# Performance work log

Hardware: AMD Instinct MI355X
Metric: run time of the kernel (lower is better)

Reference implementation:

```python
import jax, jax.numpy as jnp
import numpy as np

N, H, D, G = 8192, 512, 256, 64
TAU, LAM, ALPHA, BETA = 0.5, 0.5, 1.0, 1.0
EPS_G, EPS_L = 1e-6, 1e-5


def setup_inputs() -> dict:
    key = jax.random.key(0)
    ks = jax.random.split(key, 8)
    za = jax.random.normal(ks[0], (N, H), dtype=jnp.float32)
    zb = jax.random.normal(ks[1], (N, H), dtype=jnp.float32)
    pos = jax.random.uniform(ks[2], (N, N), dtype=jnp.float32)
    batch = (jnp.arange(N, dtype=jnp.int32) * G) // N  # sorted, covers all G groups
    s_h = np.sqrt(2.0 / H).astype(np.float32)  # kaiming fan_in relu
    W1 = jax.random.normal(ks[3], (H, H), dtype=jnp.float32) * s_h
    b1 = jnp.zeros((H,), dtype=jnp.float32)
    W2 = jax.random.normal(ks[4], (H, H), dtype=jnp.float32) * s_h
    b2 = jnp.zeros((H,), dtype=jnp.float32)
    W3 = jax.random.normal(ks[5], (H, D), dtype=jnp.float32) * s_h
    b3 = jnp.zeros((D,), dtype=jnp.float32)
    a1 = jnp.full((1,), 0.5, dtype=jnp.float32)
    g1 = jnp.ones((H,), dtype=jnp.float32)
    be1 = jnp.zeros((H,), dtype=jnp.float32)
    a2 = jnp.full((1,), 0.5, dtype=jnp.float32)
    g2 = jnp.ones((H,), dtype=jnp.float32)
    be2 = jnp.zeros((H,), dtype=jnp.float32)
    return {"za": za, "zb": zb, "pos": pos, "batch": batch,
            "W1": W1, "b1": b1, "a1": a1, "g1": g1, "be1": be1,
            "W2": W2, "b2": b2, "a2": a2, "g2": g2, "be2": be2,
            "W3": W3, "b3": b3}


def _project(z, W1, b1, a1, g1, be1, W2, b2, a2, g2, be2, W3, b3):
    h = z @ W1 + b1
    h = jnp.tanh(a1 * h) * g1 + be1  # DyT
    h = h @ W2 + b2
    h = jnp.tanh(a2 * h) * g2 + be2  # DyT
    p = h @ W3 + b3
    return p * jax.nn.sigmoid(p)  # z1_proj * sigmoid(z1_proj)


def reference(za, zb, pos, batch, W1, b1, a1, g1, be1, W2, b2, a2, g2, be2, W3, b3):
    za_p = _project(za, W1, b1, a1, g1, be1, W2, b2, a2, g2, be2, W3, b3)
    zb_p = _project(zb, W1, b1, a1, g1, be1, W2, b2, a2, g2, be2, W3, b3)

    # exp(cosine / tau): same matrix used by global_contrast (sim) and local_contrast
    na = jnp.linalg.norm(za_p, axis=-1, keepdims=True)  # [N,1]
    nb = jnp.linalg.norm(zb_p, axis=-1, keepdims=True)  # [N,1]
    m = jnp.exp((za_p @ zb_p.T) / (na * nb.T) / TAU)    # [N,N]

    # global contrast
    a2b = m / (jnp.sum(m, axis=1, keepdims=True) + EPS_G)
    lori_a = -jnp.mean(jnp.log(jnp.sum(a2b * pos, axis=-1)))
    b2a = m.T
    b2a = b2a / (jnp.sum(b2a, axis=1, keepdims=True) + EPS_G)
    lori_b = -jnp.mean(jnp.log(jnp.sum(b2a * pos, axis=-1)))
    global_loss = LAM * lori_a + (1.0 - LAM) * lori_b

    # local contrast: per-group sums via one-hot matmul (replaces O(G^2) mask loop)
    pos_sim = jnp.diagonal(m)                              # [N]
    pos_sim_graph = jax.ops.segment_sum(pos_sim, batch, num_segments=G)  # [G]
    hot = jax.nn.one_hot(batch, G, dtype=m.dtype)          # [N,G]
    batch_sim = hot.T @ m @ hot                            # [G,G]
    graph_sim = jnp.diagonal(batch_sim)
    neg0 = jnp.sum(batch_sim, axis=0) - graph_sim
    neg1 = jnp.sum(batch_sim, axis=1) - graph_sim
    loss0 = jnp.mean(jnp.log(pos_sim_graph / (neg0 + EPS_L)))
    loss1 = jnp.mean(jnp.log(pos_sim_graph / (neg1 + EPS_L)))
    inter_loss = (loss0 + loss1) / 2.0
    inner_loss = -jnp.mean(jnp.log(pos_sim_graph / (graph_sim - pos_sim_graph + EPS_L)))
    local_loss = ALPHA * inter_loss + BETA * inner_loss

    total_loss = global_loss + local_loss
    return total_loss, jnp.concatenate((za_p, zb_p), axis=1)
```

## Files before the change

### kernel.cpp

```cpp
#include <hip/hip_runtime.h>
#include <hip/hip_bf16.h>
#include <cstdint>
#include <cstddef>


typedef __bf16 bf16;
typedef __bf16 bf16x4 __attribute__((ext_vector_type(4)));
typedef __bf16 bf16x8 __attribute__((ext_vector_type(8)));
typedef float  f32x4  __attribute__((ext_vector_type(4)));

#define NROWS 8192
#define HDIM  512
#define DDIM  256
#define GGRP  64
#define INV_TAU 2.0f

__device__ __forceinline__ void async_ld16(const void* g, void* l) {
    __builtin_amdgcn_global_load_lds(
        (__attribute__((address_space(1))) void*)(g),
        (__attribute__((address_space(3))) void*)(l), 16, 0, 0);
}

__device__ __forceinline__ void mfma_tile_128(
    const bf16* __restrict__ A, const bf16* __restrict__ Bt, int K,
    int row0, int col0, bf16* ldsA, bf16* ldsB, f32x4 acc[4][4])
{
    const int tid  = threadIdx.x;
    const int lane = tid & 63;
    const int wave = tid >> 6;
    const int wrow = (wave >> 1) * 64;
    const int wcol = (wave & 1) * 64;
    const int lrow = lane & 15;
    const int lk8  = (lane >> 4) * 8;

#pragma unroll
    for (int i = 0; i < 4; i++)
#pragma unroll
        for (int j = 0; j < 4; j++) acc[i][j] = (f32x4){0.f, 0.f, 0.f, 0.f};

    for (int k0 = 0; k0 < K; k0 += 32) {
#pragma unroll
        for (int t = 0; t < 2; t++) {
            int f = t * 256 + tid;
            int r = f >> 2;
            int c = (f & 3) * 8;
            async_ld16(A  + (size_t)(row0 + r) * K + k0 + c,
                       ldsA + (size_t)(t * 256 + wave * 64) * 8);
            async_ld16(Bt + (size_t)(col0 + r) * K + k0 + c,
                       ldsB + (size_t)(t * 256 + wave * 64) * 8);
        }
        __syncthreads();

        bf16x8 af[4], bfr[4];
#pragma unroll
        for (int fi = 0; fi < 4; fi++)
            af[fi] = *(const bf16x8*)(ldsA + (wrow + fi * 16 + lrow) * 32 + lk8);
#pragma unroll
        for (int fj = 0; fj < 4; fj++)
            bfr[fj] = *(const bf16x8*)(ldsB + (wcol + fj * 16 + lrow) * 32 + lk8);
#pragma unroll
        for (int fi = 0; fi < 4; fi++)
#pragma unroll
            for (int fj = 0; fj < 4; fj++)
                acc[fi][fj] = __builtin_amdgcn_mfma_f32_16x16x32_bf16(
                    af[fi], bfr[fj], acc[fi][fj], 0, 0, 0);
        __syncthreads();
    }
}

__global__ __launch_bounds__(256) void gemm_dyt(
    const bf16* __restrict__ A, const bf16* __restrict__ Bt, bf16* __restrict__ C,
    int K, int N,
    const float* __restrict__ bias, const float* __restrict__ alph,
    const float* __restrict__ gam, const float* __restrict__ bet)
{
    __shared__ __align__(16) bf16 ldsA[128 * 32];
    __shared__ __align__(16) bf16 ldsB[128 * 32];
    f32x4 acc[4][4];
    const int row0 = blockIdx.y * 128, col0 = blockIdx.x * 128;
    mfma_tile_128(A, Bt, K, row0, col0, ldsA, ldsB, acc);

    const int lane = threadIdx.x & 63, wave = threadIdx.x >> 6;
    const int wrow = (wave >> 1) * 64, wcol = (wave & 1) * 64;
    const int lcol = lane & 15, lrg = (lane >> 4) * 4;
    const float a = alph[0];
#pragma unroll
    for (int fi = 0; fi < 4; fi++) {
        const int rbase = row0 + wrow + fi * 16 + lrg;
#pragma unroll
        for (int fj = 0; fj < 4; fj++) {
            const int cg = col0 + wcol + fj * 16 + lcol;
            const float bcol = bias[cg], gcol = gam[cg], becol = bet[cg];
#pragma unroll
            for (int r = 0; r < 4; r++) {
                float x = acc[fi][fj][r] + bcol;
                float y = tanhf(a * x) * gcol + becol;
                C[(size_t)(rbase + r) * N + cg] = (bf16)y;
            }
        }
    }
}

__global__ __launch_bounds__(256) void gemm_silu(
    const bf16* __restrict__ A, const bf16* __restrict__ Bt,
    bf16* __restrict__ P16, float* __restrict__ out1, float* __restrict__ n2,
    const float* __restrict__ bias)
{
    __shared__ __align__(16) bf16 ldsA[128 * 32];
    __shared__ __align__(16) bf16 ldsB[128 * 32];
    f32x4 acc[4][4];
    const int row0 = blockIdx.y * 128, col0 = blockIdx.x * 128;
    mfma_tile_128(A, Bt, 512, row0, col0, ldsA, ldsB, acc);

    const int lane = threadIdx.x & 63, wave = threadIdx.x >> 6;
    const int wrow = (wave >> 1) * 64, wcol = (wave & 1) * 64;
    const int lcol = lane & 15, lrg = (lane >> 4) * 4;

    float nacc[4][4];
#pragma unroll
    for (int i = 0; i < 4; i++)
#pragma unroll
        for (int r = 0; r < 4; r++) nacc[i][r] = 0.f;

#pragma unroll
    for (int fi = 0; fi < 4; fi++) {
        const int rbase = row0 + wrow + fi * 16 + lrg;
#pragma unroll
        for (int fj = 0; fj < 4; fj++) {
            const int cg = col0 + wcol + fj * 16 + lcol;
            const float bcol = bias[cg];
#pragma unroll
            for (int r = 0; r < 4; r++) {
                const int rg = rbase + r;
                float x = acc[fi][fj][r] + bcol;
                float y = x / (1.f + __expf(-x));
                P16[(size_t)rg * 256 + cg] = (bf16)y;
                size_t oidx = (rg < NROWS) ? ((size_t)rg * 512 + cg)
                                           : ((size_t)(rg - NROWS) * 512 + 256 + cg);
                out1[oidx] = y;
                nacc[fi][r] += y * y;
            }
        }
    }
#pragma unroll
    for (int fi = 0; fi < 4; fi++)
#pragma unroll
        for (int r = 0; r < 4; r++) {
            float v = nacc[fi][r];
            v += __shfl_xor(v, 1); v += __shfl_xor(v, 2);
            v += __shfl_xor(v, 4); v += __shfl_xor(v, 8);
            if (lcol == 0)
                atomicAdd(&n2[row0 + wrow + fi * 16 + lrg + r], v);
        }
}

template <int PASS1>
__global__ __launch_bounds__(256, 2) void flash_sim(
    const bf16* __restrict__ PA, const bf16* __restrict__ PB,
    const float* __restrict__ rnA, const float* __restrict__ rnB,
    const float* __restrict__ pos,
    float* __restrict__ rsum, float* __restrict__ wsum,
    float* __restrict__ bsim, float* __restrict__ psg)
{
    const int lane = threadIdx.x & 63;
    const int wave = threadIdx.x >> 6;
    const int lrow = lane & 15;
    const int lk8  = (lane >> 4) * 8;
    const int lrg  = lane >> 4;
    const int R0   = blockIdx.y * 128 + wave * 32;
    const int C0   = blockIdx.x * 1024;

    bf16x8 a[2][8];
#pragma unroll
    for (int fi = 0; fi < 2; fi++)
#pragma unroll
        for (int kk = 0; kk < 8; kk++)
            a[fi][kk] = *(const bf16x8*)(
                PA + (size_t)(R0 + fi * 16 + lrow) * DDIM + kk * 32 + lk8);

    float rna[2][4];
#pragma unroll
    for (int fi = 0; fi < 2; fi++)
#pragma unroll
        for (int r = 0; r < 4; r++)
            rna[fi][r] = rnA[R0 + fi * 16 + lrg * 4 + r] * INV_TAU;

    float racc[2][4], sacc[2][4];
#pragma unroll
    for (int fi = 0; fi < 2; fi++)
#pragma unroll
        for (int r = 0; r < 4; r++) { racc[fi][r] = 0.f; sacc[fi][r] = 0.f; }
    float msum = 0.f, dacc = 0.f;

#pragma unroll 2
    for (int ct = 0; ct < 32; ct++) {
        const int c0 = C0 + ct * 32;

        bf16x8 b[2][8];
#pragma unroll
        for (int fj = 0; fj < 2; fj++)
#pragma unroll
            for (int kk = 0; kk < 8; kk++)
                b[fj][kk] = *(const bf16x8*)(
                    PB + (size_t)(c0 + fj * 16 + lrow) * DDIM + kk * 32 + lk8);

        f32x4 acc[2][2];
#pragma unroll
        for (int fi = 0; fi < 2; fi++)
#pragma unroll
            for (int fj = 0; fj < 2; fj++) acc[fi][fj] = (f32x4){0.f, 0.f, 0.f, 0.f};
#pragma unroll
        for (int kk = 0; kk < 8; kk++)
#pragma unroll
            for (int fi = 0; fi < 2; fi++)
#pragma unroll
                for (int fj = 0; fj < 2; fj++)
                    acc[fi][fj] = __builtin_amdgcn_mfma_f32_16x16x32_bf16(
                        a[fi][kk], b[fj][kk], acc[fi][fj], 0, 0, 0);

        float rnb[2];
        rnb[0] = rnB[c0 + lrow];
        rnb[1] = rnB[c0 + 16 + lrow];

        const bool diag_tile = PASS1 && (c0 == R0);
#pragma unroll
        for (int fi = 0; fi < 2; fi++)
#pragma unroll
            for (int fj = 0; fj < 2; fj++)
#pragma unroll
                for (int r = 0; r < 4; r++) {
                    float m = __expf(acc[fi][fj][r] * rna[fi][r] * rnb[fj]);
                    float pv = pos[(size_t)(R0 + fi * 16 + lrg * 4 + r) * NROWS
                                   + c0 + fj * 16 + lrow];
                    racc[fi][r] += m;
                    sacc[fi][r] += m * pv;
                    if (PASS1) {
                        msum += m;
                        if (diag_tile &&
                            (fi * 16 + lrg * 4 + r) == (fj * 16 + lrow))
                            dacc += m;
                    }
                }

        if (PASS1 && (ct & 3) == 3) {
            float v = msum;
            v += __shfl_xor(v, 1);  v += __shfl_xor(v, 2);
            v += __shfl_xor(v, 4);  v += __shfl_xor(v, 8);
            v += __shfl_xor(v, 16); v += __shfl_xor(v, 32);
            if (lane == 0)
                atomicAdd(&bsim[blockIdx.y * GGRP + (c0 >> 7)], v);
            msum = 0.f;
        }
    }

#pragma unroll
    for (int fi = 0; fi < 2; fi++)
#pragma unroll
        for (int r = 0; r < 4; r++) {
            float rv = racc[fi][r], sv = sacc[fi][r];
            rv += __shfl_xor(rv, 1); rv += __shfl_xor(rv, 2);
            rv += __shfl_xor(rv, 4); rv += __shfl_xor(rv, 8);
            sv += __shfl_xor(sv, 1); sv += __shfl_xor(sv, 2);
            sv += __shfl_xor(sv, 4); sv += __shfl_xor(sv, 8);
            if (lrow == 0) {
                const int rg = R0 + fi * 16 + lrg * 4 + r;
                atomicAdd(&rsum[rg], rv);
                atomicAdd(&wsum[rg], sv);
            }
        }
    if (PASS1 && blockIdx.x == (unsigned)(R0 >> 10)) {
        dacc += __shfl_xor(dacc, 1);  dacc += __shfl_xor(dacc, 2);
        dacc += __shfl_xor(dacc, 4);  dacc += __shfl_xor(dacc, 8);
        dacc += __shfl_xor(dacc, 16); dacc += __shfl_xor(dacc, 32);
        if (lane == 0) atomicAdd(&psg[blockIdx.y], dacc);
    }
}

__global__ void cast4_kernel(const float4* __restrict__ x, bf16x4* __restrict__ y, int n4)
{
    int i = blockIdx.x * blockDim.x + threadIdx.x;
    if (i < n4) {
        float4 v = x[i];
        bf16x4 o;
        o[0] = (bf16)v.x; o[1] = (bf16)v.y; o[2] = (bf16)v.z; o[3] = (bf16)v.w;
        y[i] = o;
    }
}

__global__ void transpose_cast(const float* __restrict__ W, bf16* __restrict__ Wt,
                               int R, int C)
{
    __shared__ float tile[32][33];
    const int c0 = blockIdx.x * 32, r0 = blockIdx.y * 32;
    const int tx = threadIdx.x, ty = threadIdx.y;
    for (int i = ty; i < 32; i += 8)
        tile[i][tx] = W[(size_t)(r0 + i) * C + c0 + tx];
    __syncthreads();
    for (int i = ty; i < 32; i += 8)
        Wt[(size_t)(c0 + i) * R + r0 + tx] = (bf16)tile[tx][i];
}

__global__ void rsqrt_kernel(const float* __restrict__ x, float* __restrict__ y, int n)
{
    int i = blockIdx.x * blockDim.x + threadIdx.x;
    if (i < n) y[i] = rsqrtf(fmaxf(x[i], 1e-30f));
}

__global__ void loss_kernel(
    const float* __restrict__ rowsum, const float* __restrict__ colsum,
    const float* __restrict__ sa, const float* __restrict__ sb,
    const float* __restrict__ bs, const float* __restrict__ psg,
    float* __restrict__ out)
{
    __shared__ float red[8];
    const int tid = threadIdx.x;
    float la = 0.f, lb = 0.f;
    for (int i = tid; i < NROWS; i += 256) {
        la += __logf(sa[i] / (rowsum[i] + 1e-6f));
        lb += __logf(sb[i] / (colsum[i] + 1e-6f));
    }
    for (int m = 1; m < 64; m <<= 1) {
        la += __shfl_xor(la, m);
        lb += __shfl_xor(lb, m);
    }
    if ((tid & 63) == 0) { red[tid >> 6] = la; red[4 + (tid >> 6)] = lb; }
    __syncthreads();

    float l0 = 0.f, l1 = 0.f, lin = 0.f;
    if (tid < GGRP) {
        const float d = bs[tid * GGRP + tid];
        float c0 = 0.f, c1 = 0.f;
        for (int a = 0; a < GGRP; a++) { c0 += bs[a * GGRP + tid]; c1 += bs[tid * GGRP + a]; }
        const float p = psg[tid];
        l0  = __logf(p / (c0 - d + 1e-5f));
        l1  = __logf(p / (c1 - d + 1e-5f));
        lin = __logf(p / (d - p + 1e-5f));
    }
    for (int m = 1; m < 64; m <<= 1) {
        l0 += __shfl_xor(l0, m); l1 += __shfl_xor(l1, m); lin += __shfl_xor(lin, m);
    }
    if (tid == 0) {
        const float lat = red[0] + red[1] + red[2] + red[3];
        const float lbt = red[4] + red[5] + red[6] + red[7];
        const float lori_a = -lat / (float)NROWS;
        const float lori_b = -lbt / (float)NROWS;
        const float global_loss = 0.5f * (lori_a + lori_b);
        const float inter = 0.5f * (l0 + l1) / (float)GGRP;
        const float inner = -lin / (float)GGRP;
        out[0] = global_loss + inter + inner;
    }
}

extern "C" void kernel_launch(void* const* d_in, const int* in_sizes, int n_in,
                              void* d_out, int out_size, void* d_ws, size_t ws_size,
                              hipStream_t stream)
{
    const float* za  = (const float*)d_in[0];
    const float* zb  = (const float*)d_in[1];
    const float* pos = (const float*)d_in[2];
    const float* W1  = (const float*)d_in[4];
    const float* b1  = (const float*)d_in[5];
    const float* a1  = (const float*)d_in[6];
    const float* g1  = (const float*)d_in[7];
    const float* be1 = (const float*)d_in[8];
    const float* W2  = (const float*)d_in[9];
    const float* b2  = (const float*)d_in[10];
    const float* a2  = (const float*)d_in[11];
    const float* g2  = (const float*)d_in[12];
    const float* be2 = (const float*)d_in[13];
    const float* W3  = (const float*)d_in[14];
    const float* b3  = (const float*)d_in[15];
    float* out = (float*)d_out;

    char* ws = (char*)d_ws;
    float* rowsum = (float*)(ws);
    float* colsum = rowsum + 8192;
    float* s_a    = colsum + 8192;
    float* s_b    = s_a + 8192;
    float* n2     = s_b + 8192;
    float* bsim   = n2 + 16384;
    float* psg    = bsim + 4096;
    const size_t accum_bytes = (size_t)(8192 * 4 + 16384 + 4096 + 64) * 4;

    float* rn  = (float*)(ws + 213248);
    bf16* Z16  = (bf16*)(ws + 213248 + 65536);
    bf16* h1   = Z16 + (size_t)16384 * 512;
    bf16* p16  = h1 + (size_t)16384 * 512;
    bf16* W1t  = p16 + (size_t)16384 * 256;
    bf16* W2t  = W1t + (size_t)512 * 512;
    bf16* W3t  = W2t + (size_t)512 * 512;

    hipMemsetAsync(d_ws, 0, accum_bytes, stream);

    const int n4 = NROWS * HDIM / 4;
    cast4_kernel<<<n4 / 256, 256, 0, stream>>>((const float4*)za, (bf16x4*)Z16, n4);
    cast4_kernel<<<n4 / 256, 256, 0, stream>>>((const float4*)zb,
                                               (bf16x4*)(Z16 + (size_t)NROWS * HDIM), n4);
    dim3 tb(32, 8);
    transpose_cast<<<dim3(16, 16), tb, 0, stream>>>(W1, W1t, 512, 512);
    transpose_cast<<<dim3(16, 16), tb, 0, stream>>>(W2, W2t, 512, 512);
    transpose_cast<<<dim3(8, 16),  tb, 0, stream>>>(W3, W3t, 512, 256);

    gemm_dyt<<<dim3(4, 128), 256, 0, stream>>>(Z16, W1t, h1, 512, 512, b1, a1, g1, be1);
    gemm_dyt<<<dim3(4, 128), 256, 0, stream>>>(h1, W2t, Z16 , 512, 512, b2, a2, g2, be2);
    gemm_silu<<<dim3(2, 128), 256, 0, stream>>>(Z16, W3t, p16, out + 1, n2, b3);
    rsqrt_kernel<<<16384 / 256, 256, 0, stream>>>(n2, rn, 16384);

    const bf16* pa = p16;
    const bf16* pb = p16 + (size_t)NROWS * DDIM;
    flash_sim<1><<<dim3(8, 64), 256, 0, stream>>>(pa, pb, rn, rn + NROWS, pos,
                                                  rowsum, s_a, bsim, psg);
    flash_sim<0><<<dim3(8, 64), 256, 0, stream>>>(pb, pa, rn + NROWS, rn, pos,
                                                  colsum, s_b, nullptr, nullptr);

    loss_kernel<<<1, 256, 0, stream>>>(rowsum, colsum, s_a, s_b, bsim, psg, out);
}
```

Measured before the change: 749.0 us.

## Shrink GEMM tiles, raise flash_sim occupancy and prefetch pos before MFMA

Projection GEMMs move from 128x128 to 64x64 tiles, doubling the number of blocks. flash_sim splits columns into 512-wide chunks with a doubled grid and requests 4 blocks per CU. It also loads the pos values and column norms before issuing MFMAs, so their latency overlaps compute. The risk is register pressure or spills at the higher occupancy target, plus lower data reuse in the smaller GEMM tiles.

```diff
diff --git a/kernel.cpp b/kernel.cpp
--- a/kernel.cpp
+++ b/kernel.cpp
@@ -21,47 +21,41 @@
         (__attribute__((address_space(3))) void*)(l), 16, 0, 0);
 }
 
-__device__ __forceinline__ void mfma_tile_128(
+__device__ __forceinline__ void mfma_tile_64k(
     const bf16* __restrict__ A, const bf16* __restrict__ Bt, int K,
-    int row0, int col0, bf16* ldsA, bf16* ldsB, f32x4 acc[4][4])
+    int arow0, int brow0, bf16* ldsA, bf16* ldsB, f32x4 acc[2][2])
 {
     const int tid  = threadIdx.x;
     const int lane = tid & 63;
     const int wave = tid >> 6;
-    const int wrow = (wave >> 1) * 64;
-    const int wcol = (wave & 1) * 64;
+    const int wrow = (wave >> 1) * 32;
+    const int wcol = (wave & 1) * 32;
     const int lrow = lane & 15;
     const int lk8  = (lane >> 4) * 8;
-
-#pragma unroll
-    for (int i = 0; i < 4; i++)
-#pragma unroll
-        for (int j = 0; j < 4; j++) acc[i][j] = (f32x4){0.f, 0.f, 0.f, 0.f};
+    const int sr   = tid >> 2;
+    const int sc   = (tid & 3) * 8;
+
+#pragma unroll
+    for (int i = 0; i < 2; i++)
+#pragma unroll
+        for (int j = 0; j < 2; j++) acc[i][j] = (f32x4){0.f, 0.f, 0.f, 0.f};
 
     for (int k0 = 0; k0 < K; k0 += 32) {
-#pragma unroll
-        for (int t = 0; t < 2; t++) {
-            int f = t * 256 + tid;
-            int r = f >> 2;
-            int c = (f & 3) * 8;
-            async_ld16(A  + (size_t)(row0 + r) * K + k0 + c,
-                       ldsA + (size_t)(t * 256 + wave * 64) * 8);
-            async_ld16(Bt + (size_t)(col0 + r) * K + k0 + c,
-                       ldsB + (size_t)(t * 256 + wave * 64) * 8);
-        }
+        async_ld16(A  + (size_t)(arow0 + sr) * K + k0 + sc, ldsA + wave * 64 * 8);
+        async_ld16(Bt + (size_t)(brow0 + sr) * K + k0 + sc, ldsB + wave * 64 * 8);
         __syncthreads();
 
-        bf16x8 af[4], bfr[4];
-#pragma unroll
-        for (int fi = 0; fi < 4; fi++)
+        bf16x8 af[2], bfr[2];
+#pragma unroll
+        for (int fi = 0; fi < 2; fi++)
             af[fi] = *(const bf16x8*)(ldsA + (wrow + fi * 16 + lrow) * 32 + lk8);
 #pragma unroll
-        for (int fj = 0; fj < 4; fj++)
+        for (int fj = 0; fj < 2; fj++)
             bfr[fj] = *(const bf16x8*)(ldsB + (wcol + fj * 16 + lrow) * 32 + lk8);
 #pragma unroll
-        for (int fi = 0; fi < 4; fi++)
-#pragma unroll
-            for (int fj = 0; fj < 4; fj++)
+        for (int fi = 0; fi < 2; fi++)
+#pragma unroll
+            for (int fj = 0; fj < 2; fj++)
                 acc[fi][fj] = __builtin_amdgcn_mfma_f32_16x16x32_bf16(
                     af[fi], bfr[fj], acc[fi][fj], 0, 0, 0);
         __syncthreads();
@@ -74,21 +68,21 @@
     const float* __restrict__ bias, const float* __restrict__ alph,
     const float* __restrict__ gam, const float* __restrict__ bet)
 {
-    __shared__ __align__(16) bf16 ldsA[128 * 32];
-    __shared__ __align__(16) bf16 ldsB[128 * 32];
-    f32x4 acc[4][4];
-    const int row0 = blockIdx.y * 128, col0 = blockIdx.x * 128;
-    mfma_tile_128(A, Bt, K, row0, col0, ldsA, ldsB, acc);
+    __shared__ __align__(16) bf16 ldsA[64 * 32];
+    __shared__ __align__(16) bf16 ldsB[64 * 32];
+    f32x4 acc[2][2];
+    const int row0 = blockIdx.y * 64, col0 = blockIdx.x * 64;
+    mfma_tile_64k(A, Bt, K, row0, col0, ldsA, ldsB, acc);
 
     const int lane = threadIdx.x & 63, wave = threadIdx.x >> 6;
-    const int wrow = (wave >> 1) * 64, wcol = (wave & 1) * 64;
-    const int lcol = lane & 15, lrg = (lane >> 4) * 4;
+    const int wrow = (wave >> 1) * 32, wcol = (wave & 1) * 32;
+    const int lcol = lane & 15, lrg4 = (lane >> 4) * 4;
     const float a = alph[0];
 #pragma unroll
-    for (int fi = 0; fi < 4; fi++) {
-        const int rbase = row0 + wrow + fi * 16 + lrg;
-#pragma unroll
-        for (int fj = 0; fj < 4; fj++) {
+    for (int fi = 0; fi < 2; fi++) {
+        const int rbase = row0 + wrow + fi * 16 + lrg4;
+#pragma unroll
+        for (int fj = 0; fj < 2; fj++) {
             const int cg = col0 + wcol + fj * 16 + lcol;
             const float bcol = bias[cg], gcol = gam[cg], becol = bet[cg];
 #pragma unroll
@@ -106,27 +100,27 @@
     bf16* __restrict__ P16, float* __restrict__ out1, float* __restrict__ n2,
     const float* __restrict__ bias)
 {
-    __shared__ __align__(16) bf16 ldsA[128 * 32];
-    __shared__ __align__(16) bf16 ldsB[128 * 32];
-    f32x4 acc[4][4];
-    const int row0 = blockIdx.y * 128, col0 = blockIdx.x * 128;
-    mfma_tile_128(A, Bt, 512, row0, col0, ldsA, ldsB, acc);
+    __shared__ __align__(16) bf16 ldsA[64 * 32];
+    __shared__ __align__(16) bf16 ldsB[64 * 32];
+    f32x4 acc[2][2];
+    const int row0 = blockIdx.y * 64, col0 = blockIdx.x * 64;
+    mfma_tile_64k(A, Bt, 512, row0, col0, ldsA, ldsB, acc);
 
     const int lane = threadIdx.x & 63, wave = threadIdx.x >> 6;
-    const int wrow = (wave >> 1) * 64, wcol = (wave & 1) * 64;
-    const int lcol = lane & 15, lrg = (lane >> 4) * 4;
-
-    float nacc[4][4];
-#pragma unroll
-    for (int i = 0; i < 4; i++)
+    const int wrow = (wave >> 1) * 32, wcol = (wave & 1) * 32;
+    const int lcol = lane & 15, lrg4 = (lane >> 4) * 4;
+
+    float nacc[2][4];
+#pragma unroll
+    for (int i = 0; i < 2; i++)
 #pragma unroll
         for (int r = 0; r < 4; r++) nacc[i][r] = 0.f;
 
 #pragma unroll
-    for (int fi = 0; fi < 4; fi++) {
-        const int rbase = row0 + wrow + fi * 16 + lrg;
-#pragma unroll
-        for (int fj = 0; fj < 4; fj++) {
+    for (int fi = 0; fi < 2; fi++) {
+        const int rbase = row0 + wrow + fi * 16 + lrg4;
+#pragma unroll
+        for (int fj = 0; fj < 2; fj++) {
             const int cg = col0 + wcol + fj * 16 + lcol;
             const float bcol = bias[cg];
 #pragma unroll
@@ -143,19 +137,19 @@
         }
     }
 #pragma unroll
-    for (int fi = 0; fi < 4; fi++)
+    for (int fi = 0; fi < 2; fi++)
 #pragma unroll
         for (int r = 0; r < 4; r++) {
             float v = nacc[fi][r];
             v += __shfl_xor(v, 1); v += __shfl_xor(v, 2);
             v += __shfl_xor(v, 4); v += __shfl_xor(v, 8);
             if (lcol == 0)
-                atomicAdd(&n2[row0 + wrow + fi * 16 + lrg + r], v);
+                atomicAdd(&n2[row0 + wrow + fi * 16 + lrg4 + r], v);
         }
 }
 
 template <int PASS1>
-__global__ __launch_bounds__(256, 2) void flash_sim(
+__global__ __launch_bounds__(256, 4) void flash_sim(
     const bf16* __restrict__ PA, const bf16* __restrict__ PB,
     const float* __restrict__ rnA, const float* __restrict__ rnB,
     const float* __restrict__ pos,
@@ -168,7 +162,7 @@
     const int lk8  = (lane >> 4) * 8;
     const int lrg  = lane >> 4;
     const int R0   = blockIdx.y * 128 + wave * 32;
-    const int C0   = blockIdx.x * 1024;
+    const int C0   = blockIdx.x * 512;
 
     bf16x8 a[2][8];
 #pragma unroll
@@ -193,7 +187,7 @@
     float msum = 0.f, dacc = 0.f;
 
 #pragma unroll 2
-    for (int ct = 0; ct < 32; ct++) {
+    for (int ct = 0; ct < 16; ct++) {
         const int c0 = C0 + ct * 32;
 
         bf16x8 b[2][8];
@@ -204,6 +198,19 @@
                 b[fj][kk] = *(const bf16x8*)(
                     PB + (size_t)(c0 + fj * 16 + lrow) * DDIM + kk * 32 + lk8);
 
+        float pv[2][2][4];
+#pragma unroll
+        for (int fi = 0; fi < 2; fi++)
+#pragma unroll
+            for (int fj = 0; fj < 2; fj++)
+#pragma unroll
+                for (int r = 0; r < 4; r++)
+                    pv[fi][fj][r] = pos[(size_t)(R0 + fi * 16 + lrg * 4 + r) * NROWS
+                                        + c0 + fj * 16 + lrow];
+        float rnb[2];
+        rnb[0] = rnB[c0 + lrow];
+        rnb[1] = rnB[c0 + 16 + lrow];
+
         f32x4 acc[2][2];
 #pragma unroll
         for (int fi = 0; fi < 2; fi++)
@@ -218,10 +225,6 @@
                     acc[fi][fj] = __builtin_amdgcn_mfma_f32_16x16x32_bf16(
                         a[fi][kk], b[fj][kk], acc[fi][fj], 0, 0, 0);
 
-        float rnb[2];
-        rnb[0] = rnB[c0 + lrow];
-        rnb[1] = rnB[c0 + 16 + lrow];
-
         const bool diag_tile = PASS1 && (c0 == R0);
 #pragma unroll
         for (int fi = 0; fi < 2; fi++)
@@ -230,10 +233,8 @@
 #pragma unroll
                 for (int r = 0; r < 4; r++) {
                     float m = __expf(acc[fi][fj][r] * rna[fi][r] * rnb[fj]);
-                    float pv = pos[(size_t)(R0 + fi * 16 + lrg * 4 + r) * NROWS
-                                   + c0 + fj * 16 + lrow];
                     racc[fi][r] += m;
-                    sacc[fi][r] += m * pv;
+                    sacc[fi][r] += m * pv[fi][fj][r];
                     if (PASS1) {
                         msum += m;
                         if (diag_tile &&
@@ -268,7 +269,7 @@
                 atomicAdd(&wsum[rg], sv);
             }
         }
-    if (PASS1 && blockIdx.x == (unsigned)(R0 >> 10)) {
+    if (PASS1 && blockIdx.x == (unsigned)(R0 >> 9)) {
         dacc += __shfl_xor(dacc, 1);  dacc += __shfl_xor(dacc, 2);
         dacc += __shfl_xor(dacc, 4);  dacc += __shfl_xor(dacc, 8);
         dacc += __shfl_xor(dacc, 16); dacc += __shfl_xor(dacc, 32);
@@ -401,17 +402,17 @@
     transpose_cast<<<dim3(16, 16), tb, 0, stream>>>(W2, W2t, 512, 512);
     transpose_cast<<<dim3(8, 16),  tb, 0, stream>>>(W3, W3t, 512, 256);
 
-    gemm_dyt<<<dim3(4, 128), 256, 0, stream>>>(Z16, W1t, h1, 512, 512, b1, a1, g1, be1);
-    gemm_dyt<<<dim3(4, 128), 256, 0, stream>>>(h1, W2t, Z16 , 512, 512, b2, a2, g2, be2);
-    gemm_silu<<<dim3(2, 128), 256, 0, stream>>>(Z16, W3t, p16, out + 1, n2, b3);
+    gemm_dyt<<<dim3(8, 256), 256, 0, stream>>>(Z16, W1t, h1, 512, 512, b1, a1, g1, be1);
+    gemm_dyt<<<dim3(8, 256), 256, 0, stream>>>(h1, W2t, Z16 , 512, 512, b2, a2, g2, be2);
+    gemm_silu<<<dim3(4, 256), 256, 0, stream>>>(Z16, W3t, p16, out + 1, n2, b3);
     rsqrt_kernel<<<16384 / 256, 256, 0, stream>>>(n2, rn, 16384);
 
     const bf16* pa = p16;
     const bf16* pb = p16 + (size_t)NROWS * DDIM;
-    flash_sim<1><<<dim3(8, 64), 256, 0, stream>>>(pa, pb, rn, rn + NROWS, pos,
-                                                  rowsum, s_a, bsim, psg);
-    flash_sim<0><<<dim3(8, 64), 256, 0, stream>>>(pb, pa, rn + NROWS, rn, pos,
-                                                  colsum, s_b, nullptr, nullptr);
+    flash_sim<1><<<dim3(16, 64), 256, 0, stream>>>(pa, pb, rn, rn + NROWS, pos,
+                                                   rowsum, s_a, bsim, psg);
+    flash_sim<0><<<dim3(16, 64), 256, 0, stream>>>(pb, pa, rn + NROWS, rn, pos,
+                                                   colsum, s_b, nullptr, nullptr);
 
     loss_kernel<<<1, 256, 0, stream>>>(rowsum, colsum, s_a, s_b, bsim, psg, out);
 }
```

Measured after the change: 901.9 us. +20.4%, slower.
